# Performance work log

Measured on AMD Instinct MI355X. Metric: run time of the kernel, lower is better.

## Reference

```python
import jax, jax.numpy as jnp
import numpy as np

S, B, D, F, E, K = 1024, 2, 512, 2048, 8, 2


def setup_inputs() -> dict:
    key = jax.random.key(0)
    ks = jax.random.split(key, 12)
    s = lambda *sh: 1.0 / np.sqrt(sh[0])
    inp = {
        "x": jax.random.normal(ks[0], (S, B, D), dtype=jnp.float32),
        # gate: nn.Linear(d_model, n_experts)
        "Wg": jax.random.normal(ks[1], (D, E), dtype=jnp.float32) * s(D),
        "bg": jnp.zeros((E,), dtype=jnp.float32),
        # routed experts: stacked FFN params (E copies of expert)
        "W1": jax.random.normal(ks[2], (E, D, F), dtype=jnp.float32) * s(D),
        "b1": jnp.zeros((E, F), dtype=jnp.float32),
        "W2": jax.random.normal(ks[3], (E, F, D), dtype=jnp.float32) * s(F),
        "b2": jnp.zeros((E, D), dtype=jnp.float32),
        # shared expert (single FFN)
        "Ws1": jax.random.normal(ks[4], (D, F), dtype=jnp.float32) * s(D),
        "bs1": jnp.zeros((F,), dtype=jnp.float32),
        "Ws2": jax.random.normal(ks[5], (F, D), dtype=jnp.float32) * s(F),
        "bs2": jnp.zeros((D,), dtype=jnp.float32),
    }
    return inp


def reference(x, Wg, bg, W1, b1, W2, b2, Ws1, bs1, Ws2, bs2):
    # gate_logits: (S, B, E)
    gate_logits = jnp.einsum("sbd,de->sbe", x, Wg) + bg
    # top-k per token (eval mode: k = n_experts_per_token, t = 1.0)
    weights, selected = jax.lax.top_k(gate_logits, K)  # (S,B,K)
    weights = jax.nn.softmax(weights.astype(jnp.float32), axis=-1)
    # combine weights per expert: (S,B,E)
    onehot = jax.nn.one_hot(selected, E, dtype=weights.dtype)  # (S,B,K,E)
    comb = jnp.einsum("sbk,sbke->sbe", weights, onehot)
    # routed experts computed densely, combined with per-token routing weight
    h = jax.nn.relu(jnp.einsum("sbd,edf->sbef", x, W1) + b1)  # (S,B,E,F)
    y = jnp.einsum("sbef,efd->sbed", h, W2) + b2              # (S,B,E,D)
    out = jnp.einsum("sbe,sbed->sbd", comb, y)
    # shared expert, scaled by 1/k
    hs = jax.nn.relu(jnp.einsum("sbd,df->sbf", x, Ws1) + bs1)
    shared = jnp.einsum("sbf,fd->sbd", hs, Ws2) + bs2
    out = out + (1.0 / K) * shared
    return out
```

## Files before the change

kernel.cpp:

```cpp
#include <hip/hip_runtime.h>
#include <hip/hip_bf16.h>
#include <stdint.h>

#define TT 2048
#define DD 512
#define FF 2048
#define EE 8

typedef unsigned short u16;
typedef __attribute__((ext_vector_type(8))) unsigned short ushort8v;
typedef __attribute__((ext_vector_type(8))) short short8;
typedef __attribute__((ext_vector_type(4))) float float4v;

__device__ __forceinline__ u16 f2bf(float f) {
    unsigned u = __float_as_uint(f);
    u += 0x7FFF + ((u >> 16) & 1);
    return (u16)(u >> 16);
}

__device__ __forceinline__ void gl_lds16(const u16* g, u16* l) {
    __builtin_amdgcn_global_load_lds(
        (const __attribute__((address_space(1))) unsigned int*)g,
        (__attribute__((address_space(3))) unsigned int*)l, 16, 0, 0);
}

#define WS_HB   0ull
#define WS_XG   (WS_HB + 6144ull*2048*2)
#define WS_WT1  (WS_XG + 2048ull*512*2)
#define WS_RTG  (WS_WT1 + 9ull*2048*512*2)
#define WS_ME   (WS_RTG + 64)
#define WS_MW   (WS_ME + 16384)
#define WS_RT   (WS_MW + 16384)
#define WS_WROW (WS_RT + 16384)
#define WS_WT2  (WS_WROW + 16384)
#define WS_NEED (WS_WT2 + 9ull*2048*512*2)

__device__ __forceinline__ void conv_unit(int j, const float* __restrict__ srcE,
                                          const float* __restrict__ srcS,
                                          u16* __restrict__ dst,
                                          int R, int C, int shC, u16* Ls) {
    int mid = j >> 8, t2 = j & 255;
    int tr = t2 >> shC, tc = t2 & ((1 << shC) - 1);
    int r0 = tr * 64, c0 = tc * 64;
    const float* src = (mid < 8) ? srcE + (size_t)mid * R * C : srcS;
    u16* dstm = dst + (size_t)mid * R * C;
    int t = threadIdx.x;
#pragma unroll
    for (int i = 0; i < 4; ++i) {
        int rr = (t >> 4) + i * 16;
        int cc = (t & 15) * 4;
        float4v v = *(const float4v*)(src + (size_t)(r0 + rr) * C + c0 + cc);
#pragma unroll
        for (int jx = 0; jx < 4; ++jx) Ls[(cc + jx) * 72 + rr] = f2bf(v[jx]);
    }
    __syncthreads();
#pragma unroll
    for (int jj = 0; jj < 2; ++jj) {
        int slot = t + jj * 256;
        int cc = slot >> 3, r8 = (slot & 7) * 8;
        ushort8v o = *(const ushort8v*)&Ls[cc * 72 + r8];
        *(ushort8v*)(dstm + (size_t)(c0 + cc) * R + r0 + r8) = o;
    }
}

__device__ __forceinline__ void gate_wave(int t, int lane,
                                          const float* __restrict__ x,
                                          const float* __restrict__ Wg,
                                          const float* __restrict__ bg,
                                          int* __restrict__ metaE,
                                          float* __restrict__ metaW,
                                          u16* __restrict__ xg) {
    const float* xp = x + (size_t)t * DD + lane * 8;
    float4v x0 = *(const float4v*)xp;
    float4v x1 = *(const float4v*)(xp + 4);
    float xf[8] = {x0[0], x0[1], x0[2], x0[3], x1[0], x1[1], x1[2], x1[3]};
    float acc[EE] = {0.f, 0.f, 0.f, 0.f, 0.f, 0.f, 0.f, 0.f};
#pragma unroll
    for (int g = 0; g < 8; ++g) {
        const float* wp = Wg + (size_t)(lane * 8 + g) * EE;
        float4v w0 = *(const float4v*)wp;
        float4v w1 = *(const float4v*)(wp + 4);
        acc[0] += xf[g] * w0[0]; acc[1] += xf[g] * w0[1];
        acc[2] += xf[g] * w0[2]; acc[3] += xf[g] * w0[3];
        acc[4] += xf[g] * w1[0]; acc[5] += xf[g] * w1[1];
        acc[6] += xf[g] * w1[2]; acc[7] += xf[g] * w1[3];
    }
#pragma unroll
    for (int off = 1; off < 64; off <<= 1) {
#pragma unroll
        for (int e = 0; e < EE; ++e) acc[e] += __shfl_xor(acc[e], off, 64);
    }
    ushort8v xv;
#pragma unroll
    for (int jx = 0; jx < 4; ++jx) xv[jx] = f2bf(x0[jx]);
#pragma unroll
    for (int jx = 0; jx < 4; ++jx) xv[4 + jx] = f2bf(x1[jx]);
    *(ushort8v*)(xg + (size_t)t * DD + lane * 8) = xv;
    if (lane == 0) {
#pragma unroll
        for (int e = 0; e < EE; ++e) acc[e] += bg[e];
        int e0 = 0; float l0 = acc[0];
#pragma unroll
        for (int e = 1; e < EE; ++e) if (acc[e] > l0) { l0 = acc[e]; e0 = e; }
        int e1 = -1; float l1 = -3.4e38f;
#pragma unroll
        for (int e = 0; e < EE; ++e)
            if (e != e0 && acc[e] > l1) { l1 = acc[e]; e1 = e; }
        float ex = __expf(l1 - l0);
        float w0 = 1.f / (1.f + ex);
        metaE[2 * t] = e0; metaE[2 * t + 1] = e1;
        metaW[2 * t] = w0; metaW[2 * t + 1] = 1.f - w0;
    }
}

__global__ __launch_bounds__(256) void fused1_k(
    const float* __restrict__ x, const float* __restrict__ Wg,
    const float* __restrict__ bg,
    const float* __restrict__ W1, const float* __restrict__ Ws1,
    const float* __restrict__ W2, const float* __restrict__ Ws2,
    float* __restrict__ out, u16* __restrict__ xg,
    u16* __restrict__ Wt1, u16* __restrict__ Wt2,
    int* __restrict__ metaE, float* __restrict__ metaW, int nconv) {
    __shared__ __align__(16) u16 Ls[64 * 72];
    int b = blockIdx.x, tid = threadIdx.x;
    if (b < nconv) {
        if (b < 2304) conv_unit(b, W1, Ws1, Wt1, DD, FF, 5, Ls);
        else          conv_unit(b - 2304, W2, Ws2, Wt2, FF, DD, 3, Ls);
    } else if (b < nconv + 512) {
        int gb = b - nconv;
        gate_wave(gb * 4 + (tid >> 6), tid & 63, x, Wg, bg, metaE, metaW, xg);
    } else {
        int zb = b - nconv - 512;
        float* op = out + (size_t)zb * 8192;
#pragma unroll
        for (int it = 0; it < 8; ++it)
            *(float4v*)(op + it * 1024 + tid * 4) = (float4v){0.f, 0.f, 0.f, 0.f};
    }
}

__global__ __launch_bounds__(256) void conv2_k(const float* __restrict__ W2,
                                               const float* __restrict__ Ws2,
                                               u16* __restrict__ Wt2) {
    __shared__ __align__(16) u16 Ls[64 * 72];
    conv_unit(blockIdx.x, W2, Ws2, Wt2, FF, DD, 3, Ls);
}

__global__ __launch_bounds__(256) void rank_k(const int* __restrict__ metaE,
                                              const float* __restrict__ metaW,
                                              int* __restrict__ routing,
                                              int* __restrict__ rtok,
                                              float* __restrict__ wrow) {
    __shared__ __align__(16) char smem[16384];
    u16* er      = (u16*)smem;
    int* segCnt  = (int*)(smem + 8192);
    int* segBase = (int*)(smem + 10240);
    int* expTot  = (int*)(smem + 12288);
    int tid = threadIdx.x, wv = tid >> 6, lane = tid & 63;
    unsigned long long below = (lane == 0) ? 0ull : ((~0ull) >> (64 - lane));
    for (int s = wv * 16; s < wv * 16 + 16; ++s) {
        int entry = s * 64 + lane;
        int e = metaE[entry];
        int rk = 0;
#pragma unroll
        for (int ee = 0; ee < 8; ++ee) {
            unsigned long long m = __ballot(e == ee);
            if (e == ee) rk = __popcll(m & below);
            if (lane == ee) segCnt[s * 8 + ee] = __popcll(m);
        }
        er[entry] = (u16)(e | (rk << 4));
    }
    __syncthreads();
    if (tid < 8) {
        int s = 0;
        for (int g = 0; g < 64; ++g) { segBase[g * 8 + tid] = s; s += segCnt[g * 8 + tid]; }
        expTot[tid] = s;
    }
    __syncthreads();
    if (tid == 0) {
        int s = 0;
        for (int e = 0; e < 8; ++e) { int c = expTot[e]; expTot[8 + e] = s; s += c; }
    }
    __syncthreads();
    if (tid < 8) { routing[tid] = expTot[8 + tid]; routing[8 + tid] = expTot[tid]; }
    for (int i = 0; i < 16; ++i) {
        int entry = tid + i * 256;
        int v = er[entry];
        int e = v & 15, rk = v >> 4;
        int row = expTot[8 + e] + segBase[(entry >> 6) * 8 + e] + rk;
        rtok[row] = entry >> 1;
        wrow[row] = metaW[entry];
    }
}

__global__ __launch_bounds__(256) void gemmA_k(
    const u16* __restrict__ xg, const u16* __restrict__ Wt1,
    const float* __restrict__ b1, const float* __restrict__ bs1,
    const int* __restrict__ routing, const int* __restrict__ rtok,
    u16* __restrict__ hbuf) {
    __shared__ __align__(16) u16 As[2 * 64 * 32];
    __shared__ __align__(16) u16 Bs[2 * 128 * 32];
    const int* offs = routing; const int* cnt = routing + 8;
    int j = blockIdx.x, tid = threadIdx.x;
    int rt, ct, Mloc, hRowBase, rowBase; bool routed;
    const u16* Bsrc; const float* bias;
    if (j < 512) {
        rt = j >> 4; ct = j & 15; Mloc = 64; rowBase = rt * 64;
        Bsrc = Wt1 + (size_t)8 * FF * DD; bias = bs1;
        hRowBase = 4096 + rt * 64; routed = false;
    } else {
        int jr = j - 512; int e = jr & 7; int rc = jr >> 3;
        rt = rc >> 4; ct = rc & 15;
        int M = cnt[e]; if (rt * 64 >= M) return;
        Mloc = M - rt * 64; if (Mloc > 64) Mloc = 64;
        rowBase = offs[e] + rt * 64;
        Bsrc = Wt1 + (size_t)e * FF * DD; bias = b1 + e * FF;
        hRowBase = rowBase; routed = true;
    }
    int n0 = ct * 128;
    int lane = tid & 63, w = tid >> 6, ln = lane & 15, quad = lane >> 4;
    int rsub = lane >> 2;
    int chunk = ((lane & 3) ^ ((lane >> 3) & 3)) * 8;
    const u16 *Ab[2], *Bb[2][2];
    {
        int r = w * 16 + rsub;
        int tok;
        if (routed) {
            int br = rowBase + r; if (br > 4095) br = 4095;
            tok = rtok[br];
        } else tok = rowBase + r;
#pragma unroll
        for (int q = 0; q < 2; ++q) Ab[q] = xg + (size_t)tok * DD + q * 32 + chunk;
#pragma unroll
        for (int i = 0; i < 2; ++i) {
            int nl = (2 * w + i) * 16 + rsub;
#pragma unroll
            for (int q = 0; q < 2; ++q)
                Bb[i][q] = Bsrc + (size_t)(n0 + nl) * DD + q * 32 + chunk;
        }
    }
    float4v acc[2][4];
#pragma unroll
    for (int a = 0; a < 2; ++a)
#pragma unroll
        for (int b = 0; b < 4; ++b) acc[a][b] = (float4v){0.f, 0.f, 0.f, 0.f};
    for (int kt = 0; kt < 8; ++kt) {
        int k0 = kt * 64;
#pragma unroll
        for (int q = 0; q < 2; ++q) {
            gl_lds16(Ab[q] + k0, &As[q * 2048 + w * 512]);
            gl_lds16(Bb[0][q] + k0, &Bs[q * 4096 + (2 * w) * 512]);
            gl_lds16(Bb[1][q] + k0, &Bs[q * 4096 + (2 * w + 1) * 512]);
        }
        __syncthreads();
        int slot = (quad ^ ((ln >> 1) & 3)) * 8;
#pragma unroll
        for (int s = 0; s < 2; ++s) {
            short8 Af[2], Bf[4];
#pragma unroll
            for (int a = 0; a < 2; ++a)
                Af[a] = *(const short8*)&As[s * 2048 + ((w & 1) * 32 + a * 16 + ln) * 32 + slot];
#pragma unroll
            for (int b = 0; b < 4; ++b)
                Bf[b] = *(const short8*)&Bs[s * 4096 + ((w >> 1) * 64 + b * 16 + ln) * 32 + slot];
#pragma unroll
            for (int a = 0; a < 2; ++a)
#pragma unroll
                for (int b = 0; b < 4; ++b)
                    acc[a][b] = __builtin_amdgcn_mfma_f32_16x16x32_bf16(Af[a], Bf[b], acc[a][b], 0, 0, 0);
        }
        __syncthreads();
    }
#pragma unroll
    for (int b = 0; b < 4; ++b) {
        int n = n0 + (w >> 1) * 64 + b * 16 + ln;
        float bv = bias[n];
#pragma unroll
        for (int a = 0; a < 2; ++a) {
#pragma unroll
            for (int i = 0; i < 4; ++i) {
                int lr = (w & 1) * 32 + a * 16 + quad * 4 + i;
                if (lr < Mloc) {
                    float v = acc[a][b][i] + bv;
                    v = v > 0.f ? v : 0.f;
                    hbuf[(size_t)(hRowBase + lr) * FF + n] = f2bf(v);
                }
            }
        }
    }
}

__global__ __launch_bounds__(256) void gemmB_k(
    const u16* __restrict__ hbuf, const u16* __restrict__ Wt2,
    const float* __restrict__ b2, const float* __restrict__ bs2,
    const int* __restrict__ routing, const int* __restrict__ rtok,
    const float* __restrict__ wrow, float* __restrict__ out) {
    __shared__ __align__(16) u16 As[2 * 64 * 32];
    __shared__ __align__(16) u16 Bs[2 * 128 * 32];
    const int* offs = routing; const int* cnt = routing + 8;
    int j = blockIdx.x, tid = threadIdx.x;
    int rt, ct, ks, Mloc, aRowBase; bool sh;
    const u16* Bsrc; const float* bias;
    if (j < 256) {
        sh = true; rt = j >> 3; int sub = j & 7; ct = sub >> 1; ks = sub & 1;
        Mloc = 64; aRowBase = 4096 + rt * 64;
        Bsrc = Wt2 + (size_t)8 * DD * FF; bias = bs2;
    } else {
        sh = false; int jr = j - 256; int e = jr & 7; int rc = jr >> 3;
        rt = rc >> 3; ct = (rc >> 1) & 3; ks = rc & 1;
        int M = cnt[e]; if (rt * 64 >= M) return;
        Mloc = M - rt * 64; if (Mloc > 64) Mloc = 64;
        aRowBase = offs[e] + rt * 64;
        Bsrc = Wt2 + (size_t)e * DD * FF; bias = b2 + e * DD;
    }
    int n0 = ct * 128;
    int lane = tid & 63, w = tid >> 6, ln = lane & 15, quad = lane >> 4;
    int rsub = lane >> 2;
    int chunk = ((lane & 3) ^ ((lane >> 3) & 3)) * 8;
    const u16 *Ab[2], *Bb[2][2];
    {
        int r = w * 16 + rsub;
#pragma unroll
        for (int q = 0; q < 2; ++q)
            Ab[q] = hbuf + (size_t)(aRowBase + r) * FF + ks * 1024 + q * 32 + chunk;
#pragma unroll
        for (int i = 0; i < 2; ++i) {
            int nl = (2 * w + i) * 16 + rsub;
#pragma unroll
            for (int q = 0; q < 2; ++q)
                Bb[i][q] = Bsrc + (size_t)(n0 + nl) * FF + ks * 1024 + q * 32 + chunk;
        }
    }
    float4v acc[2][4];
#pragma unroll
    for (int a = 0; a < 2; ++a)
#pragma unroll
        for (int b = 0; b < 4; ++b) acc[a][b] = (float4v){0.f, 0.f, 0.f, 0.f};
    for (int kt = 0; kt < 16; ++kt) {
        int k0 = kt * 64;
#pragma unroll
        for (int q = 0; q < 2; ++q) {
            gl_lds16(Ab[q] + k0, &As[q * 2048 + w * 512]);
            gl_lds16(Bb[0][q] + k0, &Bs[q * 4096 + (2 * w) * 512]);
            gl_lds16(Bb[1][q] + k0, &Bs[q * 4096 + (2 * w + 1) * 512]);
        }
        __syncthreads();
        int slot = (quad ^ ((ln >> 1) & 3)) * 8;
#pragma unroll
        for (int s = 0; s < 2; ++s) {
            short8 Af[2], Bf[4];
#pragma unroll
            for (int a = 0; a < 2; ++a)
                Af[a] = *(const short8*)&As[s * 2048 + ((w & 1) * 32 + a * 16 + ln) * 32 + slot];
#pragma unroll
            for (int b = 0; b < 4; ++b)
                Bf[b] = *(const short8*)&Bs[s * 4096 + ((w >> 1) * 64 + b * 16 + ln) * 32 + slot];
#pragma unroll
            for (int a = 0; a < 2; ++a)
#pragma unroll
                for (int b = 0; b < 4; ++b)
                    acc[a][b] = __builtin_amdgcn_mfma_f32_16x16x32_bf16(Af[a], Bf[b], acc[a][b], 0, 0, 0);
        }
        __syncthreads();
    }
    float bv[4];
#pragma unroll
    for (int b = 0; b < 4; ++b)
        bv[b] = (ks == 0) ? bias[n0 + (w >> 1) * 64 + b * 16 + ln] : 0.f;
#pragma unroll
    for (int a = 0; a < 2; ++a) {
#pragma unroll
        for (int i = 0; i < 4; ++i) {
            int lr = (w & 1) * 32 + a * 16 + quad * 4 + i;
            if (lr < Mloc) {
                int row = aRowBase + lr;
                int t; float wr;
                if (sh) { t = row - 4096; wr = 0.5f; }
                else    { t = rtok[row]; wr = wrow[row]; }
                float* op = out + (size_t)t * DD;
#pragma unroll
                for (int b = 0; b < 4; ++b) {
                    int n = n0 + (w >> 1) * 64 + b * 16 + ln;
                    atomicAdd(op + n, wr * (acc[a][b][i] + bv[b]));
                }
            }
        }
    }
}

extern "C" void kernel_launch(void* const* d_in, const int* in_sizes, int n_in,
                              void* d_out, int out_size, void* d_ws, size_t ws_size,
                              hipStream_t stream) {
    const float* x   = (const float*)d_in[0];
    const float* Wg  = (const float*)d_in[1];
    const float* bg  = (const float*)d_in[2];
    const float* W1  = (const float*)d_in[3];
    const float* b1  = (const float*)d_in[4];
    const float* W2  = (const float*)d_in[5];
    const float* b2  = (const float*)d_in[6];
    const float* Ws1 = (const float*)d_in[7];
    const float* bs1 = (const float*)d_in[8];
    const float* Ws2 = (const float*)d_in[9];
    const float* bs2 = (const float*)d_in[10];
    float* out = (float*)d_out;

    char* ws = (char*)d_ws;
    u16*   hbuf    = (u16*)(ws + WS_HB);
    u16*   xg      = (u16*)(ws + WS_XG);
    u16*   Wt1     = (u16*)(ws + WS_WT1);
    int*   routing = (int*)(ws + WS_RTG);
    int*   metaE   = (int*)(ws + WS_ME);
    float* metaW   = (float*)(ws + WS_MW);
    int*   rtok    = (int*)(ws + WS_RT);
    float* wrow    = (float*)(ws + WS_WROW);
    bool   big     = ws_size >= WS_NEED;
    u16*   Wt2     = big ? (u16*)(ws + WS_WT2) : Wt1;
    int    nconv   = big ? 4608 : 2304;

    fused1_k<<<nconv + 640, 256, 0, stream>>>(x, Wg, bg, W1, Ws1, W2, Ws2,
                                              out, xg, Wt1, Wt2, metaE, metaW, nconv);
    rank_k<<<1, 256, 0, stream>>>(metaE, metaW, routing, rtok, wrow);
    gemmA_k<<<4608, 256, 0, stream>>>(xg, Wt1, b1, bs1, routing, rtok, hbuf);
    if (!big) conv2_k<<<2304, 256, 0, stream>>>(W2, Ws2, Wt2);
    gemmB_k<<<2304, 256, 0, stream>>>(hbuf, Wt2, b2, bs2, routing, rtok, wrow, out);
}
```

Measured before the change: 220.7 us.

## Fold routing rank into GEMM blocks and double-buffer LDS K-loop

After: 241.0 us. +9.2%, slower.

```diff
diff --git a/kernel.cpp b/kernel.cpp
--- a/kernel.cpp
+++ b/kernel.cpp
@@ -27,12 +27,9 @@
 #define WS_HB   0ull
 #define WS_XG   (WS_HB + 6144ull*2048*2)
 #define WS_WT1  (WS_XG + 2048ull*512*2)
-#define WS_RTG  (WS_WT1 + 9ull*2048*512*2)
-#define WS_ME   (WS_RTG + 64)
+#define WS_ME   (WS_WT1 + 9ull*2048*512*2)
 #define WS_MW   (WS_ME + 16384)
-#define WS_RT   (WS_MW + 16384)
-#define WS_WROW (WS_RT + 16384)
-#define WS_WT2  (WS_WROW + 16384)
+#define WS_WT2  (WS_MW + 16384)
 #define WS_NEED (WS_WT2 + 9ull*2048*512*2)
 
 __device__ __forceinline__ void conv_unit(int j, const float* __restrict__ srcE,
@@ -145,130 +142,134 @@
     conv_unit(blockIdx.x, W2, Ws2, Wt2, FF, DD, 3, Ls);
 }
 
-__global__ __launch_bounds__(256) void rank_k(const int* __restrict__ metaE,
-                                              const float* __restrict__ metaW,
-                                              int* __restrict__ routing,
-                                              int* __restrict__ rtok,
-                                              float* __restrict__ wrow) {
-    __shared__ __align__(16) char smem[16384];
-    u16* er      = (u16*)smem;
-    int* segCnt  = (int*)(smem + 8192);
-    int* segBase = (int*)(smem + 10240);
-    int* expTot  = (int*)(smem + 12288);
-    int tid = threadIdx.x, wv = tid >> 6, lane = tid & 63;
+__device__ __forceinline__ void rank_inblock(
+    const int* __restrict__ metaE, u16* er, int* scanA, int* scanB,
+    int* offs8, u16* row2ent, int tid, int w, int lane, int** prefOut) {
     unsigned long long below = (lane == 0) ? 0ull : ((~0ull) >> (64 - lane));
-    for (int s = wv * 16; s < wv * 16 + 16; ++s) {
+    for (int s = w * 16; s < w * 16 + 16; ++s) {
         int entry = s * 64 + lane;
         int e = metaE[entry];
         int rk = 0;
 #pragma unroll
-        for (int ee = 0; ee < 8; ++ee) {
-            unsigned long long m = __ballot(e == ee);
-            if (e == ee) rk = __popcll(m & below);
-            if (lane == ee) segCnt[s * 8 + ee] = __popcll(m);
+        for (int x = 0; x < 8; ++x) {
+            unsigned long long m = __ballot(e == x);
+            if (e == x) rk = __popcll(m & below);
+            if (lane == x) scanA[s * 8 + x] = __popcll(m);
         }
         er[entry] = (u16)(e | (rk << 4));
     }
     __syncthreads();
+    int* a = scanA; int* b2 = scanB;
+    for (int off = 1; off < 64; off <<= 1) {
+        for (int s = tid; s < 512; s += 256) {
+            int g = s >> 3;
+            int v = a[s] + (g >= off ? a[s - (off << 3)] : 0);
+            b2[s] = v;
+        }
+        __syncthreads();
+        int* t = a; a = b2; b2 = t;
+    }
     if (tid < 8) {
         int s = 0;
-        for (int g = 0; g < 64; ++g) { segBase[g * 8 + tid] = s; s += segCnt[g * 8 + tid]; }
-        expTot[tid] = s;
+        for (int x = 0; x < tid; ++x) s += a[504 + x];
+        offs8[tid] = s;
     }
     __syncthreads();
-    if (tid == 0) {
-        int s = 0;
-        for (int e = 0; e < 8; ++e) { int c = expTot[e]; expTot[8 + e] = s; s += c; }
-    }
-    __syncthreads();
-    if (tid < 8) { routing[tid] = expTot[8 + tid]; routing[8 + tid] = expTot[tid]; }
+    *prefOut = a;
+}
+
+__device__ __forceinline__ void rank_scatter(
+    const u16* er, const int* pref, const int* offs8, u16* row2ent, int tid) {
     for (int i = 0; i < 16; ++i) {
         int entry = tid + i * 256;
         int v = er[entry];
-        int e = v & 15, rk = v >> 4;
-        int row = expTot[8 + e] + segBase[(entry >> 6) * 8 + e] + rk;
-        rtok[row] = entry >> 1;
-        wrow[row] = metaW[entry];
+        int x = v & 15, rk = v >> 4;
+        int g = entry >> 6;
+        int base = offs8[x] + (g ? pref[(g - 1) * 8 + x] : 0);
+        row2ent[base + rk] = (u16)entry;
     }
 }
 
 __global__ __launch_bounds__(256) void gemmA_k(
     const u16* __restrict__ xg, const u16* __restrict__ Wt1,
     const float* __restrict__ b1, const float* __restrict__ bs1,
-    const int* __restrict__ routing, const int* __restrict__ rtok,
+    const int* __restrict__ metaE, const float* __restrict__ metaW,
     u16* __restrict__ hbuf) {
-    __shared__ __align__(16) u16 As[2 * 64 * 32];
-    __shared__ __align__(16) u16 Bs[2 * 128 * 32];
-    const int* offs = routing; const int* cnt = routing + 8;
+    __shared__ __align__(16) u16 As0[64 * 32];
+    __shared__ __align__(16) u16 As1[64 * 32];
+    __shared__ __align__(16) u16 Bs0[128 * 32];
+    __shared__ __align__(16) u16 Bs1[128 * 32];
     int j = blockIdx.x, tid = threadIdx.x;
-    int rt, ct, Mloc, hRowBase, rowBase; bool routed;
+    int lane = tid & 63, w = tid >> 6, ln = lane & 15, quad = lane >> 4;
+    int rsub = lane >> 2;
+    int chunk = ((lane & 3) ^ ((lane >> 3) & 3)) * 8;
+
+    int rt, ct, Mloc, hRowBase; bool routed = (j >= 512);
     const u16* Bsrc; const float* bias;
-    if (j < 512) {
-        rt = j >> 4; ct = j & 15; Mloc = 64; rowBase = rt * 64;
+    int tok;
+    if (!routed) {
+        rt = j >> 4; ct = j & 15; Mloc = 64;
         Bsrc = Wt1 + (size_t)8 * FF * DD; bias = bs1;
-        hRowBase = 4096 + rt * 64; routed = false;
+        hRowBase = 4096 + rt * 64;
+        tok = rt * 64 + w * 16 + rsub;
     } else {
         int jr = j - 512; int e = jr & 7; int rc = jr >> 3;
         rt = rc >> 4; ct = rc & 15;
-        int M = cnt[e]; if (rt * 64 >= M) return;
-        Mloc = M - rt * 64; if (Mloc > 64) Mloc = 64;
-        rowBase = offs[e] + rt * 64;
+        u16* er = Bs0; u16* row2ent = Bs1;
+        int* scanA = (int*)As0; int* scanB = scanA + 512;
+        int* offs8 = (int*)As1;
+        int* pref;
+        rank_inblock(metaE, er, scanA, scanB, offs8, row2ent, tid, w, lane, &pref);
+        int myCnt = pref[504 + e];
+        if (rt * 64 >= myCnt) return;
+        rank_scatter(er, pref, offs8, row2ent, tid);
+        __syncthreads();
+        int rowBase = offs8[e] + rt * 64;
+        Mloc = myCnt - rt * 64; if (Mloc > 64) Mloc = 64;
+        int br = rowBase + w * 16 + rsub; if (br > 4095) br = 4095;
+        tok = row2ent[br] >> 1;
+        hRowBase = rowBase;
         Bsrc = Wt1 + (size_t)e * FF * DD; bias = b1 + e * FF;
-        hRowBase = rowBase; routed = true;
+        __syncthreads();
     }
     int n0 = ct * 128;
-    int lane = tid & 63, w = tid >> 6, ln = lane & 15, quad = lane >> 4;
-    int rsub = lane >> 2;
-    int chunk = ((lane & 3) ^ ((lane >> 3) & 3)) * 8;
-    const u16 *Ab[2], *Bb[2][2];
-    {
-        int r = w * 16 + rsub;
-        int tok;
-        if (routed) {
-            int br = rowBase + r; if (br > 4095) br = 4095;
-            tok = rtok[br];
-        } else tok = rowBase + r;
-#pragma unroll
-        for (int q = 0; q < 2; ++q) Ab[q] = xg + (size_t)tok * DD + q * 32 + chunk;
-#pragma unroll
-        for (int i = 0; i < 2; ++i) {
-            int nl = (2 * w + i) * 16 + rsub;
-#pragma unroll
-            for (int q = 0; q < 2; ++q)
-                Bb[i][q] = Bsrc + (size_t)(n0 + nl) * DD + q * 32 + chunk;
-        }
-    }
+    const u16* ApA  = xg + (size_t)tok * DD + chunk;
+    const u16* ApB0 = Bsrc + (size_t)(n0 + (2 * w) * 16 + rsub) * DD + chunk;
+    const u16* ApB1 = Bsrc + (size_t)(n0 + (2 * w + 1) * 16 + rsub) * DD + chunk;
+
     float4v acc[2][4];
 #pragma unroll
     for (int a = 0; a < 2; ++a)
 #pragma unroll
         for (int b = 0; b < 4; ++b) acc[a][b] = (float4v){0.f, 0.f, 0.f, 0.f};
-    for (int kt = 0; kt < 8; ++kt) {
-        int k0 = kt * 64;
-#pragma unroll
-        for (int q = 0; q < 2; ++q) {
-            gl_lds16(Ab[q] + k0, &As[q * 2048 + w * 512]);
-            gl_lds16(Bb[0][q] + k0, &Bs[q * 4096 + (2 * w) * 512]);
-            gl_lds16(Bb[1][q] + k0, &Bs[q * 4096 + (2 * w + 1) * 512]);
-        }
-        __syncthreads();
-        int slot = (quad ^ ((ln >> 1) & 3)) * 8;
-#pragma unroll
-        for (int s = 0; s < 2; ++s) {
-            short8 Af[2], Bf[4];
-#pragma unroll
-            for (int a = 0; a < 2; ++a)
-                Af[a] = *(const short8*)&As[s * 2048 + ((w & 1) * 32 + a * 16 + ln) * 32 + slot];
-#pragma unroll
-            for (int b = 0; b < 4; ++b)
-                Bf[b] = *(const short8*)&Bs[s * 4096 + ((w >> 1) * 64 + b * 16 + ln) * 32 + slot];
-#pragma unroll
-            for (int a = 0; a < 2; ++a)
-#pragma unroll
-                for (int b = 0; b < 4; ++b)
-                    acc[a][b] = __builtin_amdgcn_mfma_f32_16x16x32_bf16(Af[a], Bf[b], acc[a][b], 0, 0, 0);
-        }
-        __syncthreads();
+
+#define STAGE_A(K0, AX, BX)                                         \
+    { gl_lds16(ApA + (K0), AX + w * 512);                           \
+      gl_lds16(ApB0 + (K0), BX + (2 * w) * 512);                    \
+      gl_lds16(ApB1 + (K0), BX + (2 * w + 1) * 512); }
+#define COMP(AX, BX)                                                \
+    { int slot = (quad ^ ((ln >> 1) & 3)) * 8;                      \
+      short8 Af[2], Bf[4];                                          \
+      _Pragma("unroll")                                             \
+      for (int a = 0; a < 2; ++a)                                   \
+          Af[a] = *(const short8*)&AX[((w & 1) * 32 + a * 16 + ln) * 32 + slot]; \
+      _Pragma("unroll")                                             \
+      for (int b = 0; b < 4; ++b)                                   \
+          Bf[b] = *(const short8*)&BX[((w >> 1) * 64 + b * 16 + ln) * 32 + slot]; \
+      _Pragma("unroll")                                             \
+      for (int a = 0; a < 2; ++a)                                   \
+          _Pragma("unroll")                                         \
+          for (int b = 0; b < 4; ++b)                               \
+              acc[a][b] = __builtin_amdgcn_mfma_f32_16x16x32_bf16(Af[a], Bf[b], acc[a][b], 0, 0, 0); }
+
+    STAGE_A(0, As0, Bs0);
+    for (int kt = 0; kt < 16; kt += 2) {
+        __syncthreads();
+        STAGE_A((kt + 1) * 32, As1, Bs1);
+        COMP(As0, Bs0);
+        __syncthreads();
+        if (kt + 2 < 16) STAGE_A((kt + 2) * 32, As0, Bs0);
+        COMP(As1, Bs1);
     }
 #pragma unroll
     for (int b = 0; b < 4; ++b) {
@@ -287,80 +288,105 @@
             }
         }
     }
+#undef STAGE_A
+#undef COMP
 }
 
 __global__ __launch_bounds__(256) void gemmB_k(
     const u16* __restrict__ hbuf, const u16* __restrict__ Wt2,
     const float* __restrict__ b2, const float* __restrict__ bs2,
-    const int* __restrict__ routing, const int* __restrict__ rtok,
-    const float* __restrict__ wrow, float* __restrict__ out) {
-    __shared__ __align__(16) u16 As[2 * 64 * 32];
-    __shared__ __align__(16) u16 Bs[2 * 128 * 32];
-    const int* offs = routing; const int* cnt = routing + 8;
+    const int* __restrict__ metaE, const float* __restrict__ metaW,
+    float* __restrict__ out) {
+    __shared__ __align__(16) u16 As0[64 * 32];
+    __shared__ __align__(16) u16 As1[64 * 32];
+    __shared__ __align__(16) u16 Bs0[128 * 32];
+    __shared__ __align__(16) u16 Bs1[128 * 32];
     int j = blockIdx.x, tid = threadIdx.x;
-    int rt, ct, ks, Mloc, aRowBase; bool sh;
-    const u16* Bsrc; const float* bias;
-    if (j < 256) {
-        sh = true; rt = j >> 3; int sub = j & 7; ct = sub >> 1; ks = sub & 1;
-        Mloc = 64; aRowBase = 4096 + rt * 64;
-        Bsrc = Wt2 + (size_t)8 * DD * FF; bias = bs2;
-    } else {
-        sh = false; int jr = j - 256; int e = jr & 7; int rc = jr >> 3;
-        rt = rc >> 3; ct = (rc >> 1) & 3; ks = rc & 1;
-        int M = cnt[e]; if (rt * 64 >= M) return;
-        Mloc = M - rt * 64; if (Mloc > 64) Mloc = 64;
-        aRowBase = offs[e] + rt * 64;
-        Bsrc = Wt2 + (size_t)e * DD * FF; bias = b2 + e * DD;
-    }
-    int n0 = ct * 128;
     int lane = tid & 63, w = tid >> 6, ln = lane & 15, quad = lane >> 4;
     int rsub = lane >> 2;
     int chunk = ((lane & 3) ^ ((lane >> 3) & 3)) * 8;
-    const u16 *Ab[2], *Bb[2][2];
+
+    int rt, ct, ks, Mloc, aRowBase; bool sh = (j < 256);
+    const u16* Bsrc; const float* bias;
+    int tokv[8]; float wrv[8];
+    if (sh) {
+        rt = j >> 3; int sub = j & 7; ct = sub >> 1; ks = sub & 1;
+        Mloc = 64; aRowBase = 4096 + rt * 64;
+        Bsrc = Wt2 + (size_t)8 * DD * FF; bias = bs2;
+#pragma unroll
+        for (int a = 0; a < 2; ++a)
+#pragma unroll
+            for (int i = 0; i < 4; ++i) {
+                int row = aRowBase + (w & 1) * 32 + a * 16 + quad * 4 + i;
+                tokv[a * 4 + i] = row - 4096; wrv[a * 4 + i] = 0.5f;
+            }
+    } else {
+        int jr = j - 256; int e = jr & 7; int rc = jr >> 3;
+        rt = rc >> 3; ct = (rc >> 1) & 3; ks = rc & 1;
+        u16* er = Bs0; u16* row2ent = Bs1;
+        int* scanA = (int*)As0; int* scanB = scanA + 512;
+        int* offs8 = (int*)As1;
+        int* pref;
+        rank_inblock(metaE, er, scanA, scanB, offs8, row2ent, tid, w, lane, &pref);
+        int myCnt = pref[504 + e];
+        if (rt * 64 >= myCnt) return;
+        rank_scatter(er, pref, offs8, row2ent, tid);
+        __syncthreads();
+        aRowBase = offs8[e] + rt * 64;
+        Mloc = myCnt - rt * 64; if (Mloc > 64) Mloc = 64;
+#pragma unroll
+        for (int a = 0; a < 2; ++a)
+#pragma unroll
+            for (int i = 0; i < 4; ++i) {
+                int row = aRowBase + (w & 1) * 32 + a * 16 + quad * 4 + i;
+                if (row > 4095) row = 4095;
+                int ent = row2ent[row];
+                tokv[a * 4 + i] = ent >> 1;
+                wrv[a * 4 + i] = metaW[ent];
+            }
+        Bsrc = Wt2 + (size_t)e * DD * FF; bias = b2 + e * DD;
+        __syncthreads();
+    }
+    int n0 = ct * 128;
     {
-        int r = w * 16 + rsub;
-#pragma unroll
-        for (int q = 0; q < 2; ++q)
-            Ab[q] = hbuf + (size_t)(aRowBase + r) * FF + ks * 1024 + q * 32 + chunk;
-#pragma unroll
-        for (int i = 0; i < 2; ++i) {
-            int nl = (2 * w + i) * 16 + rsub;
-#pragma unroll
-            for (int q = 0; q < 2; ++q)
-                Bb[i][q] = Bsrc + (size_t)(n0 + nl) * FF + ks * 1024 + q * 32 + chunk;
-        }
-    }
+    }
+    const u16* ApA = hbuf + (size_t)(aRowBase + w * 16 + rsub) * FF + ks * 1024 + chunk;
+    const u16* ApB0 = Bsrc + (size_t)(n0 + (2 * w) * 16 + rsub) * FF + ks * 1024 + chunk;
+    const u16* ApB1 = Bsrc + (size_t)(n0 + (2 * w + 1) * 16 + rsub) * FF + ks * 1024 + chunk;
+
     float4v acc[2][4];
 #pragma unroll
     for (int a = 0; a < 2; ++a)
 #pragma unroll
         for (int b = 0; b < 4; ++b) acc[a][b] = (float4v){0.f, 0.f, 0.f, 0.f};
-    for (int kt = 0; kt < 16; ++kt) {
-        int k0 = kt * 64;
-#pragma unroll
-        for (int q = 0; q < 2; ++q) {
-            gl_lds16(Ab[q] + k0, &As[q * 2048 + w * 512]);
-            gl_lds16(Bb[0][q] + k0, &Bs[q * 4096 + (2 * w) * 512]);
-            gl_lds16(Bb[1][q] + k0, &Bs[q * 4096 + (2 * w + 1) * 512]);
-        }
-        __syncthreads();
-        int slot = (quad ^ ((ln >> 1) & 3)) * 8;
-#pragma unroll
-        for (int s = 0; s < 2; ++s) {
-            short8 Af[2], Bf[4];
-#pragma unroll
-            for (int a = 0; a < 2; ++a)
-                Af[a] = *(const short8*)&As[s * 2048 + ((w & 1) * 32 + a * 16 + ln) * 32 + slot];
-#pragma unroll
-            for (int b = 0; b < 4; ++b)
-                Bf[b] = *(const short8*)&Bs[s * 4096 + ((w >> 1) * 64 + b * 16 + ln) * 32 + slot];
-#pragma unroll
-            for (int a = 0; a < 2; ++a)
-#pragma unroll
-                for (int b = 0; b < 4; ++b)
-                    acc[a][b] = __builtin_amdgcn_mfma_f32_16x16x32_bf16(Af[a], Bf[b], acc[a][b], 0, 0, 0);
-        }
-        __syncthreads();
+
+#define STAGE_B(K0, AX, BX)                                         \
+    { gl_lds16(ApA + (K0), AX + w * 512);                           \
+      gl_lds16(ApB0 + (K0), BX + (2 * w) * 512);                    \
+      gl_lds16(ApB1 + (K0), BX + (2 * w + 1) * 512); }
+#define COMP(AX, BX)                                                \
+    { int slot = (quad ^ ((ln >> 1) & 3)) * 8;                      \
+      short8 Af[2], Bf[4];                                          \
+      _Pragma("unroll")                                             \
+      for (int a = 0; a < 2; ++a)                                   \
+          Af[a] = *(const short8*)&AX[((w & 1) * 32 + a * 16 + ln) * 32 + slot]; \
+      _Pragma("unroll")                                             \
+      for (int b = 0; b < 4; ++b)                                   \
+          Bf[b] = *(const short8*)&BX[((w >> 1) * 64 + b * 16 + ln) * 32 + slot]; \
+      _Pragma("unroll")                                             \
+      for (int a = 0; a < 2; ++a)                                   \
+          _Pragma("unroll")                                         \
+          for (int b = 0; b < 4; ++b)                               \
+              acc[a][b] = __builtin_amdgcn_mfma_f32_16x16x32_bf16(Af[a], Bf[b], acc[a][b], 0, 0, 0); }
+
+    STAGE_B(0, As0, Bs0);
+    for (int kt = 0; kt < 32; kt += 2) {
+        __syncthreads();
+        STAGE_B((kt + 1) * 32, As1, Bs1);
+        COMP(As0, Bs0);
+        __syncthreads();
+        if (kt + 2 < 32) STAGE_B((kt + 2) * 32, As0, Bs0);
+        COMP(As1, Bs1);
     }
     float bv[4];
 #pragma unroll
@@ -372,11 +398,8 @@
         for (int i = 0; i < 4; ++i) {
             int lr = (w & 1) * 32 + a * 16 + quad * 4 + i;
             if (lr < Mloc) {
-                int row = aRowBase + lr;
-                int t; float wr;
-                if (sh) { t = row - 4096; wr = 0.5f; }
-                else    { t = rtok[row]; wr = wrow[row]; }
-                float* op = out + (size_t)t * DD;
+                float* op = out + (size_t)tokv[a * 4 + i] * DD;
+                float wr = wrv[a * 4 + i];
 #pragma unroll
                 for (int b = 0; b < 4; ++b) {
                     int n = n0 + (w >> 1) * 64 + b * 16 + ln;
@@ -385,6 +408,8 @@
             }
         }
     }
+#undef STAGE_B
+#undef COMP
 }
 
 extern "C" void kernel_launch(void* const* d_in, const int* in_sizes, int n_in,
@@ -404,22 +429,18 @@
     float* out = (float*)d_out;
 
     char* ws = (char*)d_ws;
-    u16*   hbuf    = (u16*)(ws + WS_HB);
-    u16*   xg      = (u16*)(ws + WS_XG);
-    u16*   Wt1     = (u16*)(ws + WS_WT1);
-    int*   routing = (int*)(ws + WS_RTG);
-    int*   metaE   = (int*)(ws + WS_ME);
-    float* metaW   = (float*)(ws + WS_MW);
-    int*   rtok    = (int*)(ws + WS_RT);
-    float* wrow    = (float*)(ws + WS_WROW);
-    bool   big     = ws_size >= WS_NEED;
-    u16*   Wt2     = big ? (u16*)(ws + WS_WT2) : Wt1;
-    int    nconv   = big ? 4608 : 2304;
+    u16*   hbuf  = (u16*)(ws + WS_HB);
+    u16*   xg    = (u16*)(ws + WS_XG);
+    u16*   Wt1   = (u16*)(ws + WS_WT1);
+    int*   metaE = (int*)(ws + WS_ME);
+    float* metaW = (float*)(ws + WS_MW);
+    bool   big   = ws_size >= WS_NEED;
+    u16*   Wt2   = big ? (u16*)(ws + WS_WT2) : Wt1;
+    int    nconv = big ? 4608 : 2304;
 
     fused1_k<<<nconv + 640, 256, 0, stream>>>(x, Wg, bg, W1, Ws1, W2, Ws2,
                                               out, xg, Wt1, Wt2, metaE, metaW, nconv);
-    rank_k<<<1, 256, 0, stream>>>(metaE, metaW, routing, rtok, wrow);
-    gemmA_k<<<4608, 256, 0, stream>>>(xg, Wt1, b1, bs1, routing, rtok, hbuf);
+    gemmA_k<<<4608, 256, 0, stream>>>(xg, Wt1, b1, bs1, metaE, metaW, hbuf);
     if (!big) conv2_k<<<2304, 256, 0, stream>>>(W2, Ws2, Wt2);
-    gemmB_k<<<2304, 256, 0, stream>>>(hbuf, Wt2, b2, bs2, routing, rtok, wrow, out);
-}
+    gemmB_k<<<2304, 256, 0, stream>>>(hbuf, Wt2, b2, bs2, metaE, metaW, out);
+}
```

## Fold routing rank into first kernel, compact GEMM job lists, move W2 conversion

Applied to the files above, without the earlier changes.

Measured after the change: 235.2 us. 1.07x slower.

```diff
diff --git a/kernel.cpp b/kernel.cpp
--- a/kernel.cpp
+++ b/kernel.cpp
@@ -27,12 +27,15 @@
 #define WS_HB   0ull
 #define WS_XG   (WS_HB + 6144ull*2048*2)
 #define WS_WT1  (WS_XG + 2048ull*512*2)
-#define WS_RTG  (WS_WT1 + 9ull*2048*512*2)
-#define WS_ME   (WS_RTG + 64)
+#define WS_ME   (WS_WT1 + 9ull*2048*512*2)
 #define WS_MW   (WS_ME + 16384)
 #define WS_RT   (WS_MW + 16384)
 #define WS_WROW (WS_RT + 16384)
-#define WS_WT2  (WS_WROW + 16384)
+#define WS_RTG  (WS_WROW + 16384)
+#define WS_JA   (WS_RTG + 128)
+#define WS_JB   (WS_JA + 8192)
+#define WS_GD   (WS_JB + 4096)
+#define WS_WT2  (WS_GD + 64)
 #define WS_NEED (WS_WT2 + 9ull*2048*512*2)
 
 __device__ __forceinline__ void conv_unit(int j, const float* __restrict__ srcE,
@@ -108,8 +111,10 @@
             if (e != e0 && acc[e] > l1) { l1 = acc[e]; e1 = e; }
         float ex = __expf(l1 - l0);
         float w0 = 1.f / (1.f + ex);
-        metaE[2 * t] = e0; metaE[2 * t + 1] = e1;
-        metaW[2 * t] = w0; metaW[2 * t + 1] = 1.f - w0;
+        atomicExch(&metaE[2 * t], e0);
+        atomicExch(&metaE[2 * t + 1], e1);
+        atomicExch(&metaW[2 * t], w0);
+        atomicExch(&metaW[2 * t + 1], 1.f - w0);
     }
 }
 
@@ -117,24 +122,90 @@
     const float* __restrict__ x, const float* __restrict__ Wg,
     const float* __restrict__ bg,
     const float* __restrict__ W1, const float* __restrict__ Ws1,
-    const float* __restrict__ W2, const float* __restrict__ Ws2,
-    float* __restrict__ out, u16* __restrict__ xg,
-    u16* __restrict__ Wt1, u16* __restrict__ Wt2,
-    int* __restrict__ metaE, float* __restrict__ metaW, int nconv) {
-    __shared__ __align__(16) u16 Ls[64 * 72];
+    float* __restrict__ out, u16* __restrict__ xg, u16* __restrict__ Wt1,
+    int* __restrict__ metaE, float* __restrict__ metaW,
+    int* __restrict__ rtok, float* __restrict__ wrow,
+    int* __restrict__ routing, int* __restrict__ jobA, int* __restrict__ jobB,
+    int* __restrict__ gateDone) {
+    __shared__ __align__(16) char smem[16384];
     int b = blockIdx.x, tid = threadIdx.x;
-    if (b < nconv) {
-        if (b < 2304) conv_unit(b, W1, Ws1, Wt1, DD, FF, 5, Ls);
-        else          conv_unit(b - 2304, W2, Ws2, Wt2, FF, DD, 3, Ls);
-    } else if (b < nconv + 512) {
-        int gb = b - nconv;
+    if (b < 2304) {
+        conv_unit(b, W1, Ws1, Wt1, DD, FF, 5, (u16*)smem);
+    } else if (b < 2816) {
+        int gb = b - 2304;
         gate_wave(gb * 4 + (tid >> 6), tid & 63, x, Wg, bg, metaE, metaW, xg);
-    } else {
-        int zb = b - nconv - 512;
+        __syncthreads();
+        if (tid == 0) { __threadfence(); atomicAdd(gateDone, 1); }
+    } else if (b < 2944) {
+        int zb = b - 2816;
         float* op = out + (size_t)zb * 8192;
 #pragma unroll
         for (int it = 0; it < 8; ++it)
             *(float4v*)(op + it * 1024 + tid * 4) = (float4v){0.f, 0.f, 0.f, 0.f};
+    } else {
+        if (tid == 0) {
+            while (atomicAdd(gateDone, 0) < 512) __builtin_amdgcn_s_sleep(8);
+            __threadfence();
+        }
+        __syncthreads();
+        u16* er      = (u16*)smem;
+        int* segCnt  = (int*)(smem + 8192);
+        int* segBase = (int*)(smem + 10240);
+        int* expTot  = (int*)(smem + 12288);
+        int wv = tid >> 6, lane = tid & 63;
+        unsigned long long below = (lane == 0) ? 0ull : ((~0ull) >> (64 - lane));
+        for (int s = wv * 16; s < wv * 16 + 16; ++s) {
+            int entry = s * 64 + lane;
+            int e = metaE[entry];
+            int rk = 0;
+#pragma unroll
+            for (int ee = 0; ee < 8; ++ee) {
+                unsigned long long m = __ballot(e == ee);
+                if (e == ee) rk = __popcll(m & below);
+                if (lane == ee) segCnt[s * 8 + ee] = __popcll(m);
+            }
+            er[entry] = (u16)(e | (rk << 4));
+        }
+        __syncthreads();
+        if (tid < 8) {
+            int s = 0;
+            for (int g = 0; g < 64; ++g) { segBase[g * 8 + tid] = s; s += segCnt[g * 8 + tid]; }
+            expTot[tid] = s;
+        }
+        __syncthreads();
+        if (tid == 0) {
+            int s = 0;
+            for (int e = 0; e < 8; ++e) { int c = expTot[e]; expTot[8 + e] = s; s += c; }
+        }
+        __syncthreads();
+        if (tid < 8) { routing[tid] = expTot[8 + tid]; routing[8 + tid] = expTot[tid]; }
+        for (int i = 0; i < 16; ++i) {
+            int entry = tid + i * 256;
+            int v = er[entry];
+            int e = v & 15, rk = v >> 4;
+            int row = expTot[8 + e] + segBase[(entry >> 6) * 8 + e] + rk;
+            rtok[row] = entry >> 1;
+            wrow[row] = metaW[entry];
+        }
+        __shared__ int nrt[8], baseA[8], baseB[8];
+        if (tid == 0) {
+            int sA = 0, sB = 0;
+            for (int e = 0; e < 8; ++e) {
+                int r = (expTot[e] + 63) >> 6;
+                nrt[e] = r; baseA[e] = sA; baseB[e] = sB;
+                sA += r * 16; sB += r * 8;
+            }
+            routing[16] = sA; routing[17] = sB;
+        }
+        __syncthreads();
+        for (int e = 0; e < 8; ++e) {
+            int nA = nrt[e] * 16;
+            for (int i = tid; i < nA; i += 256)
+                jobA[baseA[e] + i] = e | ((i >> 4) << 3) | ((i & 15) << 9);
+            int nB = nrt[e] * 8;
+            for (int i = tid; i < nB; i += 256)
+                jobB[baseB[e] + i] = e | ((i >> 3) << 3) | ((i & 7) << 9);
+        }
     }
 }
 
@@ -145,74 +216,35 @@
     conv_unit(blockIdx.x, W2, Ws2, Wt2, FF, DD, 3, Ls);
 }
 
-__global__ __launch_bounds__(256) void rank_k(const int* __restrict__ metaE,
-                                              const float* __restrict__ metaW,
-                                              int* __restrict__ routing,
-                                              int* __restrict__ rtok,
-                                              float* __restrict__ wrow) {
-    __shared__ __align__(16) char smem[16384];
-    u16* er      = (u16*)smem;
-    int* segCnt  = (int*)(smem + 8192);
-    int* segBase = (int*)(smem + 10240);
-    int* expTot  = (int*)(smem + 12288);
-    int tid = threadIdx.x, wv = tid >> 6, lane = tid & 63;
-    unsigned long long below = (lane == 0) ? 0ull : ((~0ull) >> (64 - lane));
-    for (int s = wv * 16; s < wv * 16 + 16; ++s) {
-        int entry = s * 64 + lane;
-        int e = metaE[entry];
-        int rk = 0;
-#pragma unroll
-        for (int ee = 0; ee < 8; ++ee) {
-            unsigned long long m = __ballot(e == ee);
-            if (e == ee) rk = __popcll(m & below);
-            if (lane == ee) segCnt[s * 8 + ee] = __popcll(m);
-        }
-        er[entry] = (u16)(e | (rk << 4));
-    }
-    __syncthreads();
-    if (tid < 8) {
-        int s = 0;
-        for (int g = 0; g < 64; ++g) { segBase[g * 8 + tid] = s; s += segCnt[g * 8 + tid]; }
-        expTot[tid] = s;
-    }
-    __syncthreads();
-    if (tid == 0) {
-        int s = 0;
-        for (int e = 0; e < 8; ++e) { int c = expTot[e]; expTot[8 + e] = s; s += c; }
-    }
-    __syncthreads();
-    if (tid < 8) { routing[tid] = expTot[8 + tid]; routing[8 + tid] = expTot[tid]; }
-    for (int i = 0; i < 16; ++i) {
-        int entry = tid + i * 256;
-        int v = er[entry];
-        int e = v & 15, rk = v >> 4;
-        int row = expTot[8 + e] + segBase[(entry >> 6) * 8 + e] + rk;
-        rtok[row] = entry >> 1;
-        wrow[row] = metaW[entry];
-    }
-}
-
 __global__ __launch_bounds__(256) void gemmA_k(
     const u16* __restrict__ xg, const u16* __restrict__ Wt1,
     const float* __restrict__ b1, const float* __restrict__ bs1,
     const int* __restrict__ routing, const int* __restrict__ rtok,
-    u16* __restrict__ hbuf) {
+    const int* __restrict__ jobA, u16* __restrict__ hbuf,
+    const float* __restrict__ W2, const float* __restrict__ Ws2,
+    u16* __restrict__ Wt2, int doConv2) {
     __shared__ __align__(16) u16 As[2 * 64 * 32];
     __shared__ __align__(16) u16 Bs[2 * 128 * 32];
-    const int* offs = routing; const int* cnt = routing + 8;
     int j = blockIdx.x, tid = threadIdx.x;
+    if (j < 2304) {
+        if (doConv2) conv_unit(j, W2, Ws2, Wt2, FF, DD, 3, As);
+        return;
+    }
     int rt, ct, Mloc, hRowBase, rowBase; bool routed;
     const u16* Bsrc; const float* bias;
-    if (j < 512) {
-        rt = j >> 4; ct = j & 15; Mloc = 64; rowBase = rt * 64;
+    if (j < 2816) {
+        int idx = j - 2304;
+        rt = idx >> 4; ct = idx & 15; Mloc = 64; rowBase = rt * 64;
         Bsrc = Wt1 + (size_t)8 * FF * DD; bias = bs1;
         hRowBase = 4096 + rt * 64; routed = false;
     } else {
-        int jr = j - 512; int e = jr & 7; int rc = jr >> 3;
-        rt = rc >> 4; ct = rc & 15;
-        int M = cnt[e]; if (rt * 64 >= M) return;
+        int idx = j - 2816;
+        if (idx >= routing[16]) return;
+        int v = jobA[idx];
+        int e = v & 7; rt = (v >> 3) & 63; ct = v >> 9;
+        int M = routing[8 + e];
+        rowBase = routing[e] + rt * 64;
         Mloc = M - rt * 64; if (Mloc > 64) Mloc = 64;
-        rowBase = offs[e] + rt * 64;
         Bsrc = Wt1 + (size_t)e * FF * DD; bias = b1 + e * FF;
         hRowBase = rowBase; routed = true;
     }
@@ -293,10 +325,10 @@
     const u16* __restrict__ hbuf, const u16* __restrict__ Wt2,
     const float* __restrict__ b2, const float* __restrict__ bs2,
     const int* __restrict__ routing, const int* __restrict__ rtok,
-    const float* __restrict__ wrow, float* __restrict__ out) {
+    const float* __restrict__ wrow, const int* __restrict__ jobB,
+    float* __restrict__ out) {
     __shared__ __align__(16) u16 As[2 * 64 * 32];
     __shared__ __align__(16) u16 Bs[2 * 128 * 32];
-    const int* offs = routing; const int* cnt = routing + 8;
     int j = blockIdx.x, tid = threadIdx.x;
     int rt, ct, ks, Mloc, aRowBase; bool sh;
     const u16* Bsrc; const float* bias;
@@ -305,11 +337,15 @@
         Mloc = 64; aRowBase = 4096 + rt * 64;
         Bsrc = Wt2 + (size_t)8 * DD * FF; bias = bs2;
     } else {
-        sh = false; int jr = j - 256; int e = jr & 7; int rc = jr >> 3;
-        rt = rc >> 3; ct = (rc >> 1) & 3; ks = rc & 1;
-        int M = cnt[e]; if (rt * 64 >= M) return;
+        sh = false;
+        int idx = j - 256;
+        if (idx >= routing[17]) return;
+        int v = jobB[idx];
+        int e = v & 7; rt = (v >> 3) & 63; int sub = v >> 9;
+        ct = sub >> 1; ks = sub & 1;
+        int M = routing[8 + e];
+        aRowBase = routing[e] + rt * 64;
         Mloc = M - rt * 64; if (Mloc > 64) Mloc = 64;
-        aRowBase = offs[e] + rt * 64;
         Bsrc = Wt2 + (size_t)e * DD * FF; bias = b2 + e * DD;
     }
     int n0 = ct * 128;
@@ -407,19 +443,24 @@
     u16*   hbuf    = (u16*)(ws + WS_HB);
     u16*   xg      = (u16*)(ws + WS_XG);
     u16*   Wt1     = (u16*)(ws + WS_WT1);
-    int*   routing = (int*)(ws + WS_RTG);
     int*   metaE   = (int*)(ws + WS_ME);
     float* metaW   = (float*)(ws + WS_MW);
     int*   rtok    = (int*)(ws + WS_RT);
     float* wrow    = (float*)(ws + WS_WROW);
+    int*   routing = (int*)(ws + WS_RTG);
+    int*   jobA    = (int*)(ws + WS_JA);
+    int*   jobB    = (int*)(ws + WS_JB);
+    int*   gateDone = (int*)(ws + WS_GD);
     bool   big     = ws_size >= WS_NEED;
     u16*   Wt2     = big ? (u16*)(ws + WS_WT2) : Wt1;
-    int    nconv   = big ? 4608 : 2304;
-
-    fused1_k<<<nconv + 640, 256, 0, stream>>>(x, Wg, bg, W1, Ws1, W2, Ws2,
-                                              out, xg, Wt1, Wt2, metaE, metaW, nconv);
-    rank_k<<<1, 256, 0, stream>>>(metaE, metaW, routing, rtok, wrow);
-    gemmA_k<<<4608, 256, 0, stream>>>(xg, Wt1, b1, bs1, routing, rtok, hbuf);
+
+    hipMemsetAsync(gateDone, 0, 4, stream);
+    fused1_k<<<2945, 256, 0, stream>>>(x, Wg, bg, W1, Ws1, out, xg, Wt1,
+                                       metaE, metaW, rtok, wrow,
+                                       routing, jobA, jobB, gateDone);
+    gemmA_k<<<4864, 256, 0, stream>>>(xg, Wt1, b1, bs1, routing, rtok, jobA, hbuf,
+                                      W2, Ws2, Wt2, big ? 1 : 0);
     if (!big) conv2_k<<<2304, 256, 0, stream>>>(W2, Ws2, Wt2);
-    gemmB_k<<<2304, 256, 0, stream>>>(hbuf, Wt2, b2, bs2, routing, rtok, wrow, out);
-}
+    gemmB_k<<<1280, 256, 0, stream>>>(hbuf, Wt2, b2, bs2, routing, rtok, wrow,
+                                      jobB, out);
+}
```
